# Optimization experiments

Measured on AMD Instinct MI355X. Metric: run time of the kernel, lower is better.

Reference implementation:

```python
import jax, jax.numpy as jnp
import numpy as np

CHUNK = 128      # chunk_size
NUM_BITS = 6     # log2(num_experts=64)


def setup_inputs() -> dict:
    key = jax.random.key(0)
    k1, k2, k3 = jax.random.split(key, 3)
    B, L, D, E = 4, 4096, 1024, 64
    x = jax.random.normal(k1, (B, L, D), dtype=jnp.float32)
    expert_weights = jax.random.normal(k2, (E, D, D), dtype=jnp.float32) * 0.02
    hyperplanes = jax.random.normal(k3, (D, NUM_BITS), dtype=jnp.float32)
    return {"x": x, "expert_weights": expert_weights, "hyperplanes": hyperplanes}


def reference(x, expert_weights, hyperplanes):
    # x: [B, L, D]; L divisible by CHUNK (no padding path taken)
    B, L, D = x.shape
    C = L // CHUNK
    xr = x.reshape(B, C, CHUNK, D)

    # --- LSH (SimHash) router, chunk-level ---
    chunk_emb = xr.mean(axis=2)                      # [B, C, D]
    proj = chunk_emb @ hyperplanes                   # [B, C, bits]
    bits = (proj > 0).astype(jnp.int32)
    powers = (2 ** jnp.arange(NUM_BITS)).astype(jnp.int32)
    e1 = jnp.sum(bits * powers, axis=-1)             # [B, C]
    weakest = jnp.argmin(jnp.abs(proj), axis=-1)     # weakest hyperplane bit
    flip = (2 ** weakest).astype(jnp.int32)
    e2 = jnp.bitwise_xor(e1, flip)                   # second expert: flip weakest bit
    # gates are all 1.0 and router_threshold=0.0 -> confidence_mask = 1.0

    # --- per-chunk expert weight gather + bmm combine (top-2 average) ---
    out = jnp.zeros_like(xr)
    for idx in (e1, e2):
        w = expert_weights[idx]                      # [B, C, D, D] gathered
        out = out + jnp.einsum('bcld,bcde->bcle', xr, w)
    out = out * 0.5
    # dropout p=0.0 / eval -> identity
    return out.reshape(B, L, D)
```

## Files before the change

kernel.cpp:

```cpp
#include <hip/hip_runtime.h>
#include <hip/hip_bf16.h>


#define BD 4
#define LD 4096
#define DD 1024
#define ED 64
#define CHUNKD 128
#define NBITS 6
#define NCHUNK 128

typedef __bf16 bf16_8 __attribute__((ext_vector_type(8)));
typedef __bf16 bf16_4 __attribute__((ext_vector_type(4)));
typedef float floatx4 __attribute__((ext_vector_type(4)));

__global__ __launch_bounds__(256) void router_kernel(
    const float* __restrict__ x, const float* __restrict__ hyp,
    int* __restrict__ eidx)
{
    const int chunk = blockIdx.x;
    const int t = threadIdx.x;
    const float* xc = x + (size_t)chunk * CHUNKD * DD;

    double cs[4] = {0.0, 0.0, 0.0, 0.0};
    for (int tok = 0; tok < CHUNKD; ++tok) {
        const float* row = xc + tok * DD;
        #pragma unroll
        for (int i = 0; i < 4; ++i) cs[i] += (double)row[t + i * 256];
    }
    double pj[NBITS];
    #pragma unroll
    for (int j = 0; j < NBITS; ++j) pj[j] = 0.0;
    #pragma unroll
    for (int i = 0; i < 4; ++i) {
        const int d = t + i * 256;
        const double emb = cs[i] * (1.0 / 128.0);
        #pragma unroll
        for (int j = 0; j < NBITS; ++j)
            pj[j] += emb * (double)hyp[d * NBITS + j];
    }
    #pragma unroll
    for (int off = 32; off > 0; off >>= 1) {
        #pragma unroll
        for (int j = 0; j < NBITS; ++j)
            pj[j] += __shfl_down(pj[j], off, 64);
    }
    __shared__ double red[4][NBITS];
    const int wave = t >> 6, lane = t & 63;
    if (lane == 0) {
        #pragma unroll
        for (int j = 0; j < NBITS; ++j) red[wave][j] = pj[j];
    }
    __syncthreads();
    if (t == 0) {
        int e1 = 0, weakest = 0;
        double best = 1e300;
        #pragma unroll
        for (int j = 0; j < NBITS; ++j) {
            double p = red[0][j] + red[1][j] + red[2][j] + red[3][j];
            if (p > 0.0) e1 |= (1 << j);
            double a = fabs(p);
            if (a < best) { best = a; weakest = j; }
        }
        eidx[chunk * 2 + 0] = e1;
        eidx[chunk * 2 + 1] = e1 ^ (1 << weakest);
    }
}

__global__ __launch_bounds__(256) void cvt_x_kernel(
    const float* __restrict__ x, __bf16* __restrict__ a)
{
    const size_t i = ((size_t)blockIdx.x * 256 + threadIdx.x) * 4;
    const float4 v = *(const float4*)(x + i);
    bf16_4 o;
    o[0] = (__bf16)v.x; o[1] = (__bf16)v.y; o[2] = (__bf16)v.z; o[3] = (__bf16)v.w;
    *(bf16_4*)(a + i) = o;
}

__global__ __launch_bounds__(256) void ffn_gemm(
    const __bf16* __restrict__ Abf,
    const float* __restrict__ W,
    const int* __restrict__ eidx,
    float* __restrict__ out)
{
    __shared__ __bf16 Als[128 * 32];
    __shared__ __bf16 Bls[128 * 32];

    const int bx = blockIdx.x;
    const int chunk = bx >> 3;
    const int n0 = (bx & 7) * 128;
    const int t = threadIdx.x;
    const int lane = t & 63;
    const int wave = t >> 6;
    const int wm = wave >> 1;
    const int wn = wave & 1;
    const int lr = lane & 15;
    const int q  = lane >> 4;

    const int e0 = eidx[chunk * 2 + 0];
    const int e1 = eidx[chunk * 2 + 1];
    const int ee[2] = {e0, e1};

    const __bf16* Ag = Abf + (size_t)chunk * CHUNKD * DD;
    const int a_col = (lane & 3) * 8;
    const int a_rsub = lane >> 2;

    floatx4 acc[4][4] = {};

    for (int xp = 0; xp < 2; ++xp) {
        const float* We = W + (size_t)ee[xp] * (DD * DD) + n0;
        for (int k0 = 0; k0 < DD; k0 += 32) {
            float bv[2][8];
            #pragma unroll
            for (int rep = 0; rep < 2; ++rep) {
                const int nb = wave * 16 + lr + rep * 64;
                const float* src = We + (size_t)(k0 + q * 8) * DD + nb;
                #pragma unroll
                for (int j = 0; j < 8; ++j) bv[rep][j] = src[(size_t)j * DD];
            }
            #pragma unroll
            for (int i = 0; i < 2; ++i) {
                const __bf16* ga = Ag + (size_t)((wave * 2 + i) * 16 + a_rsub) * DD + k0 + a_col;
                __builtin_amdgcn_global_load_lds(
                    (const __attribute__((address_space(1))) void*)ga,
                    (__attribute__((address_space(3))) void*)(&Als[(wave * 2 + i) * 512]),
                    16, 0, 0);
            }
            #pragma unroll
            for (int rep = 0; rep < 2; ++rep) {
                const int nb = wave * 16 + lr + rep * 64;
                bf16_8 bw;
                #pragma unroll
                for (int j = 0; j < 8; ++j) bw[j] = (__bf16)bv[rep][j];
                *(bf16_8*)(&Bls[nb * 32 + q * 8]) = bw;
            }
            __syncthreads();

            bf16_8 af[4], bf[4];
            #pragma unroll
            for (int mt = 0; mt < 4; ++mt)
                af[mt] = *(const bf16_8*)(&Als[(wm * 64 + mt * 16 + lr) * 32 + q * 8]);
            #pragma unroll
            for (int nt = 0; nt < 4; ++nt)
                bf[nt] = *(const bf16_8*)(&Bls[(wn * 64 + nt * 16 + lr) * 32 + q * 8]);
            #pragma unroll
            for (int mt = 0; mt < 4; ++mt) {
                #pragma unroll
                for (int nt = 0; nt < 4; ++nt)
                    acc[mt][nt] = __builtin_amdgcn_mfma_f32_16x16x32_bf16(
                        af[mt], bf[nt], acc[mt][nt], 0, 0, 0);
            }
            __syncthreads();
        }
    }

    const size_t orow0 = (size_t)chunk * CHUNKD;
    #pragma unroll
    for (int mt = 0; mt < 4; ++mt) {
        #pragma unroll
        for (int nt = 0; nt < 4; ++nt) {
            const int col = n0 + wn * 64 + nt * 16 + lr;
            #pragma unroll
            for (int r = 0; r < 4; ++r) {
                const int row = wm * 64 + mt * 16 + q * 4 + r;
                out[(orow0 + row) * DD + col] = acc[mt][nt][r] * 0.5f;
            }
        }
    }
}

extern "C" void kernel_launch(void* const* d_in, const int* in_sizes, int n_in,
                              void* d_out, int out_size, void* d_ws, size_t ws_size,
                              hipStream_t stream) {
    const float* x   = (const float*)d_in[0];
    const float* W   = (const float*)d_in[1];
    const float* hyp = (const float*)d_in[2];
    float* out = (float*)d_out;

    int* eidx = (int*)d_ws;
    __bf16* Abf = (__bf16*)((char*)d_ws + 1024);

    router_kernel<<<NCHUNK, 256, 0, stream>>>(x, hyp, eidx);
    cvt_x_kernel<<<(BD * LD * DD) / (256 * 4), 256, 0, stream>>>(x, Abf);
    ffn_gemm<<<NCHUNK * 8, 256, 0, stream>>>(Abf, W, eidx, out);
}
```

Baseline: 584.8 us.

## Pre-convert expert weights to transposed bf16 and fuse router sum with x conversion

Adds a pass that converts all 64 expert weight matrices to bf16 in a transposed [n][k] layout, so the GEMM can stream B tiles straight into LDS with global_load_lds instead of doing strided fp32 loads and converting in registers. It also fuses the per-chunk column sum into the x-to-bf16 conversion through double-precision atomics, leaving a lighter router kernel. The weight conversion reads all 256MB of fp32 weights every call, even though only the routed experts are used. The new path runs only if the workspace is large enough, and the old path is kept as a fallback.

```diff
diff --git a/kernel.cpp b/kernel.cpp
--- a/kernel.cpp
+++ b/kernel.cpp
@@ -14,27 +14,43 @@
 typedef __bf16 bf16_4 __attribute__((ext_vector_type(4)));
 typedef float floatx4 __attribute__((ext_vector_type(4)));
 
-__global__ __launch_bounds__(256) void router_kernel(
-    const float* __restrict__ x, const float* __restrict__ hyp,
+__global__ __launch_bounds__(256) void sum_cvt_kernel(
+    const float* __restrict__ x, __bf16* __restrict__ a, double* __restrict__ csum)
+{
+    const int chunk = blockIdx.x >> 3;
+    const int tg = blockIdx.x & 7;
+    const size_t base = (size_t)chunk * CHUNKD * DD + (size_t)tg * 16 * DD;
+    const float* xc = x + base;
+    __bf16* ac = a + base;
+    const int t = threadIdx.x;
+
+    double s0 = 0, s1 = 0, s2 = 0, s3 = 0;
+    #pragma unroll 4
+    for (int tok = 0; tok < 16; ++tok) {
+        const float4 v = *(const float4*)(xc + tok * DD + t * 4);
+        bf16_4 o;
+        o[0] = (__bf16)v.x; o[1] = (__bf16)v.y; o[2] = (__bf16)v.z; o[3] = (__bf16)v.w;
+        *(bf16_4*)(ac + tok * DD + t * 4) = o;
+        s0 += (double)v.x; s1 += (double)v.y; s2 += (double)v.z; s3 += (double)v.w;
+    }
+    double* c = csum + (size_t)chunk * DD + t * 4;
+    atomicAdd(c + 0, s0); atomicAdd(c + 1, s1);
+    atomicAdd(c + 2, s2); atomicAdd(c + 3, s3);
+}
+
+__global__ __launch_bounds__(256) void router2_kernel(
+    const double* __restrict__ csum, const float* __restrict__ hyp,
     int* __restrict__ eidx)
 {
     const int chunk = blockIdx.x;
     const int t = threadIdx.x;
-    const float* xc = x + (size_t)chunk * CHUNKD * DD;
-
-    double cs[4] = {0.0, 0.0, 0.0, 0.0};
-    for (int tok = 0; tok < CHUNKD; ++tok) {
-        const float* row = xc + tok * DD;
-        #pragma unroll
-        for (int i = 0; i < 4; ++i) cs[i] += (double)row[t + i * 256];
-    }
     double pj[NBITS];
     #pragma unroll
     for (int j = 0; j < NBITS; ++j) pj[j] = 0.0;
     #pragma unroll
     for (int i = 0; i < 4; ++i) {
         const int d = t + i * 256;
-        const double emb = cs[i] * (1.0 / 128.0);
+        const double emb = csum[(size_t)chunk * DD + d] * (1.0 / 128.0);
         #pragma unroll
         for (int j = 0; j < NBITS; ++j)
             pj[j] += emb * (double)hyp[d * NBITS + j];
@@ -59,27 +75,40 @@
         for (int j = 0; j < NBITS; ++j) {
             double p = red[0][j] + red[1][j] + red[2][j] + red[3][j];
             if (p > 0.0) e1 |= (1 << j);
-            double a = fabs(p);
-            if (a < best) { best = a; weakest = j; }
+            double aa = fabs(p);
+            if (aa < best) { best = aa; weakest = j; }
         }
         eidx[chunk * 2 + 0] = e1;
         eidx[chunk * 2 + 1] = e1 ^ (1 << weakest);
     }
 }
 
-__global__ __launch_bounds__(256) void cvt_x_kernel(
-    const float* __restrict__ x, __bf16* __restrict__ a)
-{
-    const size_t i = ((size_t)blockIdx.x * 256 + threadIdx.x) * 4;
-    const float4 v = *(const float4*)(x + i);
-    bf16_4 o;
-    o[0] = (__bf16)v.x; o[1] = (__bf16)v.y; o[2] = (__bf16)v.z; o[3] = (__bf16)v.w;
-    *(bf16_4*)(a + i) = o;
-}
-
-__global__ __launch_bounds__(256) void ffn_gemm(
+__global__ __launch_bounds__(256) void wcvt_kernel(
+    const float* __restrict__ W, __bf16* __restrict__ Wt)
+{
+    const int e = blockIdx.x >> 4;
+    const int n0 = (blockIdx.x & 15) * 64;
+    const float* We = W + (size_t)e * DD * DD;
+    __bf16* Wte = Wt + (size_t)e * DD * DD;
+    const int nl = threadIdx.x & 63;
+    const int kc = threadIdx.x >> 6;
+    const int n = n0 + nl;
+
+    for (int it = 0; it < 32; ++it) {
+        const int k = it * 32 + kc * 8;
+        float v[8];
+        #pragma unroll
+        for (int j = 0; j < 8; ++j) v[j] = We[(size_t)(k + j) * DD + n];
+        bf16_8 o;
+        #pragma unroll
+        for (int j = 0; j < 8; ++j) o[j] = (__bf16)v[j];
+        *(bf16_8*)(&Wte[(size_t)n * DD + k]) = o;
+    }
+}
+
+__global__ __launch_bounds__(256) void ffn_gemm_bf16(
     const __bf16* __restrict__ Abf,
-    const float* __restrict__ W,
+    const __bf16* __restrict__ Wt,
     const int* __restrict__ eidx,
     float* __restrict__ out)
 {
@@ -97,16 +126,149 @@
     const int lr = lane & 15;
     const int q  = lane >> 4;
 
-    const int e0 = eidx[chunk * 2 + 0];
-    const int e1 = eidx[chunk * 2 + 1];
-    const int ee[2] = {e0, e1};
-
+    const int ee[2] = {eidx[chunk * 2 + 0], eidx[chunk * 2 + 1]};
+
+    const __bf16* Ag = Abf + (size_t)chunk * CHUNKD * DD;
+
+    floatx4 acc[4][4] = {};
+
+    for (int xp = 0; xp < 2; ++xp) {
+        const __bf16* Bg = Wt + (size_t)ee[xp] * (DD * DD) + (size_t)n0 * DD;
+        for (int k0 = 0; k0 < DD; k0 += 32) {
+            #pragma unroll
+            for (int i = 0; i < 2; ++i) {
+                const int rb = wave * 2 + i;
+                const __bf16* ga = Ag + (size_t)(rb * 16 + lr) * DD + k0 + q * 8;
+                __builtin_amdgcn_global_load_lds(
+                    (const __attribute__((address_space(1))) void*)ga,
+                    (__attribute__((address_space(3))) void*)(&Als[rb * 512]),
+                    16, 0, 0);
+            }
+            #pragma unroll
+            for (int i = 0; i < 2; ++i) {
+                const int rb = wave * 2 + i;
+                const __bf16* gb = Bg + (size_t)(rb * 16 + lr) * DD + k0 + q * 8;
+                __builtin_amdgcn_global_load_lds(
+                    (const __attribute__((address_space(1))) void*)gb,
+                    (__attribute__((address_space(3))) void*)(&Bls[rb * 512]),
+                    16, 0, 0);
+            }
+            __syncthreads();
+
+            bf16_8 af[4], bfr[4];
+            #pragma unroll
+            for (int mt = 0; mt < 4; ++mt)
+                af[mt] = *(const bf16_8*)(&Als[(wm * 4 + mt) * 512 + lane * 8]);
+            #pragma unroll
+            for (int nt = 0; nt < 4; ++nt)
+                bfr[nt] = *(const bf16_8*)(&Bls[(wn * 4 + nt) * 512 + lane * 8]);
+            #pragma unroll
+            for (int mt = 0; mt < 4; ++mt) {
+                #pragma unroll
+                for (int nt = 0; nt < 4; ++nt)
+                    acc[mt][nt] = __builtin_amdgcn_mfma_f32_16x16x32_bf16(
+                        af[mt], bfr[nt], acc[mt][nt], 0, 0, 0);
+            }
+            __syncthreads();
+        }
+    }
+
+    const size_t orow0 = (size_t)chunk * CHUNKD;
+    #pragma unroll
+    for (int mt = 0; mt < 4; ++mt) {
+        #pragma unroll
+        for (int nt = 0; nt < 4; ++nt) {
+            const int col = n0 + wn * 64 + nt * 16 + lr;
+            #pragma unroll
+            for (int r = 0; r < 4; ++r) {
+                const int row = wm * 64 + mt * 16 + q * 4 + r;
+                out[(orow0 + row) * DD + col] = acc[mt][nt][r] * 0.5f;
+            }
+        }
+    }
+}
+
+__global__ __launch_bounds__(256) void router_kernel(
+    const float* __restrict__ x, const float* __restrict__ hyp,
+    int* __restrict__ eidx)
+{
+    const int chunk = blockIdx.x;
+    const int t = threadIdx.x;
+    const float* xc = x + (size_t)chunk * CHUNKD * DD;
+    double cs[4] = {0.0, 0.0, 0.0, 0.0};
+    for (int tok = 0; tok < CHUNKD; ++tok) {
+        const float* row = xc + tok * DD;
+        #pragma unroll
+        for (int i = 0; i < 4; ++i) cs[i] += (double)row[t + i * 256];
+    }
+    double pj[NBITS];
+    #pragma unroll
+    for (int j = 0; j < NBITS; ++j) pj[j] = 0.0;
+    #pragma unroll
+    for (int i = 0; i < 4; ++i) {
+        const int d = t + i * 256;
+        const double emb = cs[i] * (1.0 / 128.0);
+        #pragma unroll
+        for (int j = 0; j < NBITS; ++j) pj[j] += emb * (double)hyp[d * NBITS + j];
+    }
+    #pragma unroll
+    for (int off = 32; off > 0; off >>= 1) {
+        #pragma unroll
+        for (int j = 0; j < NBITS; ++j) pj[j] += __shfl_down(pj[j], off, 64);
+    }
+    __shared__ double red[4][NBITS];
+    const int wave = t >> 6, lane = t & 63;
+    if (lane == 0) {
+        #pragma unroll
+        for (int j = 0; j < NBITS; ++j) red[wave][j] = pj[j];
+    }
+    __syncthreads();
+    if (t == 0) {
+        int e1 = 0, weakest = 0;
+        double best = 1e300;
+        #pragma unroll
+        for (int j = 0; j < NBITS; ++j) {
+            double p = red[0][j] + red[1][j] + red[2][j] + red[3][j];
+            if (p > 0.0) e1 |= (1 << j);
+            double a = fabs(p);
+            if (a < best) { best = a; weakest = j; }
+        }
+        eidx[chunk * 2 + 0] = e1;
+        eidx[chunk * 2 + 1] = e1 ^ (1 << weakest);
+    }
+}
+
+__global__ __launch_bounds__(256) void cvt_x_kernel(
+    const float* __restrict__ x, __bf16* __restrict__ a)
+{
+    const size_t i = ((size_t)blockIdx.x * 256 + threadIdx.x) * 4;
+    const float4 v = *(const float4*)(x + i);
+    bf16_4 o;
+    o[0] = (__bf16)v.x; o[1] = (__bf16)v.y; o[2] = (__bf16)v.z; o[3] = (__bf16)v.w;
+    *(bf16_4*)(a + i) = o;
+}
+
+__global__ __launch_bounds__(256) void ffn_gemm_fp32w(
+    const __bf16* __restrict__ Abf, const float* __restrict__ W,
+    const int* __restrict__ eidx, float* __restrict__ out)
+{
+    __shared__ __bf16 Als[128 * 32];
+    __shared__ __bf16 Bls[128 * 32];
+    const int bx = blockIdx.x;
+    const int chunk = bx >> 3;
+    const int n0 = (bx & 7) * 128;
+    const int t = threadIdx.x;
+    const int lane = t & 63;
+    const int wave = t >> 6;
+    const int wm = wave >> 1;
+    const int wn = wave & 1;
+    const int lr = lane & 15;
+    const int q  = lane >> 4;
+    const int ee[2] = {eidx[chunk * 2 + 0], eidx[chunk * 2 + 1]};
     const __bf16* Ag = Abf + (size_t)chunk * CHUNKD * DD;
     const int a_col = (lane & 3) * 8;
     const int a_rsub = lane >> 2;
-
     floatx4 acc[4][4] = {};
-
     for (int xp = 0; xp < 2; ++xp) {
         const float* We = W + (size_t)ee[xp] * (DD * DD) + n0;
         for (int k0 = 0; k0 < DD; k0 += 32) {
@@ -135,25 +297,23 @@
                 *(bf16_8*)(&Bls[nb * 32 + q * 8]) = bw;
             }
             __syncthreads();
-
-            bf16_8 af[4], bf[4];
+            bf16_8 af[4], bfr[4];
             #pragma unroll
             for (int mt = 0; mt < 4; ++mt)
                 af[mt] = *(const bf16_8*)(&Als[(wm * 64 + mt * 16 + lr) * 32 + q * 8]);
             #pragma unroll
             for (int nt = 0; nt < 4; ++nt)
-                bf[nt] = *(const bf16_8*)(&Bls[(wn * 64 + nt * 16 + lr) * 32 + q * 8]);
+                bfr[nt] = *(const bf16_8*)(&Bls[(wn * 64 + nt * 16 + lr) * 32 + q * 8]);
             #pragma unroll
             for (int mt = 0; mt < 4; ++mt) {
                 #pragma unroll
                 for (int nt = 0; nt < 4; ++nt)
                     acc[mt][nt] = __builtin_amdgcn_mfma_f32_16x16x32_bf16(
-                        af[mt], bf[nt], acc[mt][nt], 0, 0, 0);
+                        af[mt], bfr[nt], acc[mt][nt], 0, 0, 0);
             }
             __syncthreads();
         }
     }
-
     const size_t orow0 = (size_t)chunk * CHUNKD;
     #pragma unroll
     for (int mt = 0; mt < 4; ++mt) {
@@ -177,10 +337,27 @@
     const float* hyp = (const float*)d_in[2];
     float* out = (float*)d_out;
 
-    int* eidx = (int*)d_ws;
-    __bf16* Abf = (__bf16*)((char*)d_ws + 1024);
-
-    router_kernel<<<NCHUNK, 256, 0, stream>>>(x, hyp, eidx);
-    cvt_x_kernel<<<(BD * LD * DD) / (256 * 4), 256, 0, stream>>>(x, Abf);
-    ffn_gemm<<<NCHUNK * 8, 256, 0, stream>>>(Abf, W, eidx, out);
-}
+    const size_t off_eidx = 0;
+    const size_t off_csum = 4096;
+    const size_t off_a    = off_csum + (size_t)NCHUNK * DD * 8;
+    const size_t off_wt   = off_a + (size_t)NCHUNK * CHUNKD * DD * 2;
+    const size_t need     = off_wt + (size_t)ED * DD * DD * 2;
+
+    int* eidx = (int*)((char*)d_ws + off_eidx);
+    __bf16* Abf = (__bf16*)((char*)d_ws + off_a);
+
+    if (ws_size >= need) {
+        double* csum = (double*)((char*)d_ws + off_csum);
+        __bf16* Wtb = (__bf16*)((char*)d_ws + off_wt);
+        hipMemsetAsync(csum, 0, (size_t)NCHUNK * DD * 8, stream);
+        sum_cvt_kernel<<<NCHUNK * 8, 256, 0, stream>>>(x, Abf, csum);
+        wcvt_kernel<<<ED * 16, 256, 0, stream>>>(W, Wtb);
+        router2_kernel<<<NCHUNK, 256, 0, stream>>>(csum, hyp, eidx);
+        ffn_gemm_bf16<<<NCHUNK * 8, 256, 0, stream>>>(Abf, Wtb, eidx, out);
+    } else {
+        __bf16* Abf2 = (__bf16*)((char*)d_ws + 1024);
+        router_kernel<<<NCHUNK, 256, 0, stream>>>(x, hyp, eidx);
+        cvt_x_kernel<<<(BD * LD * DD) / (256 * 4), 256, 0, stream>>>(x, Abf2);
+        ffn_gemm_fp32w<<<NCHUNK * 8, 256, 0, stream>>>(Abf2, W, eidx, out);
+    }
+}
```

New measurement: 642.1 us. 9.8% more time.
